# Kernel tuning notes

Hardware: AMD Instinct MI355X
Metric: run time of the kernel (lower is better)

## Reference

```python
import jax, jax.numpy as jnp
import numpy as np

NUM_IMU = 72
NUM_NOISE = 12
MAX_PROP = 300
LN_EPS = 1e-5

def _softplus(x):
    return jax.nn.softplus(x)

def setup_inputs() -> dict:
    key = jax.random.key(0)
    k1, k2, k3, k4, k5 = jax.random.split(key, 5)
    d_model = 1024
    seq_len = 4096
    hidden_states = jax.random.normal(k1, (1, seq_len, d_model), dtype=jnp.float32)
    ln_gamma = jnp.ones((d_model,), dtype=jnp.float32)
    ln_beta = jnp.zeros((d_model,), dtype=jnp.float32)
    # Linear: d_model -> NUM_IMU * NUM_NOISE
    W = jax.random.normal(k2, (d_model, NUM_IMU * NUM_NOISE), dtype=jnp.float32) / np.sqrt(d_model)
    b = jax.random.normal(k3, (NUM_IMU * NUM_NOISE,), dtype=jnp.float32) * 0.01
    return {"hidden_states": hidden_states, "ln_gamma": ln_gamma, "ln_beta": ln_beta, "W": W, "b": b}

def _forward(hidden_states, ln_gamma, ln_beta, W, b):
    seq_len = hidden_states.shape[1]
    tsteps = min(MAX_PROP, seq_len)
    x = hidden_states[0]  # [seq, d_model] (squeeze batch=1)
    mu = jnp.mean(x, axis=-1, keepdims=True)
    var = jnp.mean((x - mu) ** 2, axis=-1, keepdims=True)
    xn = (x - mu) * jax.lax.rsqrt(var + LN_EPS) * ln_gamma + ln_beta
    # noise params: [seq, NUM_NOISE, NUM_IMU]
    p = (xn @ W + b).reshape(seq_len, NUM_NOISE, NUM_IMU)
    c = p[:, 4, :]
    c_theta = p[:, 5, :]
    phi = p[:, 6, :]
    phi_theta = p[:, 7, :]
    d = _softplus(p[:, 1, :])
    k = d ** 2 / 4 + _softplus(p[:, 0, :])
    d_theta = _softplus(p[:, 3, :])
    k_theta = d_theta ** 2 / 4 + _softplus(p[:, 2, :])
    acc_base = p[:, 8, :].T      # [imu, seq]
    acc_std = _softplus(p[:, 9, :]).T
    gyro_base = p[:, 10, :].T
    gyro_std = _softplus(p[:, 11, :]).T
    # vectorize over imu: move to [imu, seq, 1]
    def I(a):
        return a.T[:, :, None]
    t = jnp.arange(tsteps, dtype=jnp.float32)[None, None, :]  # [1,1,tstep]
    k_, d_, phi_, c_ = I(k), I(d), I(phi), I(c)
    kt_, dt_, pht_, ct_ = I(k_theta), I(d_theta), I(phi_theta), I(c_theta)
    omega1 = jnp.sqrt(k_ * 4 - d_ ** 2) / 2
    lin = c_ * jnp.exp(-d_ / 2 * t) * jnp.sin(t * omega1 + phi_)
    omega2 = jnp.sqrt(kt_ * 4 - dt_ ** 2) / 2
    ang = ct_ * jnp.exp(-dt_ / 2 * t) * jnp.sin(t * omega2 + pht_)
    spring = lin + ang  # [imu, seq, tstep]
    # banded scatter-add: out[s+t] += spring[:, s, t] for s+t < seq_len
    pos = jnp.arange(seq_len, dtype=jnp.int32)[:, None] + jnp.arange(tsteps, dtype=jnp.int32)[None, :]
    pos_flat = pos.reshape(-1)
    mask = pos_flat < seq_len
    pos_safe = jnp.where(mask, pos_flat, 0)
    vals = spring.reshape(NUM_IMU, -1) * mask.astype(spring.dtype)
    kinematics = jnp.zeros((NUM_IMU, seq_len), dtype=spring.dtype).at[:, pos_safe].add(vals)
    return kinematics, acc_base, acc_std, gyro_base, gyro_std

def reference(hidden_states, ln_gamma, ln_beta, W, b):
    return _forward(hidden_states, ln_gamma, ln_beta, W, b)
```

## Files before the change

### kernel.cpp

```cpp
#include <hip/hip_runtime.h>
#include <hip/hip_bf16.h>
#include <math.h>

#define SEQ 4096
#define DM  1024
#define NIMU 72
#define NNOISE 12
#define NJ (NIMU*NNOISE)
#define TSTEPS 300
#define PLANE (NIMU*SEQ)

#define A2F_SHORTS ((size_t)256 * 64 * 512)
#define BTF_SHORTS ((size_t)56 * 64 * 512)

typedef __attribute__((ext_vector_type(8))) short bf16x8;
typedef __attribute__((ext_vector_type(4))) float f32x4;
typedef __attribute__((ext_vector_type(2))) float f32x2;

__device__ __forceinline__ float softplus_f(float x) {
    return fmaxf(x, 0.f) + log1pf(expf(-fabsf(x)));
}

__device__ __forceinline__ void split_bf16(float x, short& hi, short& lo) {
    unsigned b = __float_as_uint(x);
    unsigned h = (b + 0x7FFFu + ((b >> 16) & 1u)) >> 16;
    float hf = __uint_as_float(h << 16);
    float r = x - hf;
    unsigned b2 = __float_as_uint(r);
    unsigned l2 = (b2 + 0x7FFFu + ((b2 >> 16) & 1u)) >> 16;
    hi = (short)h;
    lo = (short)l2;
}

__global__ __launch_bounds__(256) void ln_kernel(const float* __restrict__ x,
                                                 const float* __restrict__ gamma,
                                                 const float* __restrict__ beta,
                                                 short* __restrict__ A2f) {
    const int s_tile = blockIdx.x;
    const int tid = threadIdx.x;
    const int mrow = tid >> 4;
    const int g    = tid & 15;
    const int row  = s_tile * 16 + mrow;
    const float4* xr = (const float4*)(x + (size_t)row * DM);

    float s = 0.f, sq = 0.f;
    #pragma unroll
    for (int i = 0; i < 16; ++i) {
        float4 v = xr[g + 16 * i];
        s  += v.x + v.y + v.z + v.w;
        sq += v.x*v.x + v.y*v.y + v.z*v.z + v.w*v.w;
    }
    #pragma unroll
    for (int off = 1; off < 16; off <<= 1) {
        s  += __shfl_xor(s, off);
        sq += __shfl_xor(sq, off);
    }
    const float mean = s * (1.f / DM);
    const float var  = sq * (1.f / DM) - mean * mean;
    const float rstd = rsqrtf(fmaxf(var, 0.f) + 1e-5f);

    #pragma unroll
    for (int i = 0; i < 16; ++i) {
        float4 v = xr[g + 16 * i];
        float4 gm = ((const float4*)gamma)[g + 16 * i];
        float4 bt = ((const float4*)beta)[g + 16 * i];
        float o[4];
        o[0] = (v.x - mean) * rstd * gm.x + bt.x;
        o[1] = (v.y - mean) * rstd * gm.y + bt.y;
        o[2] = (v.z - mean) * rstd * gm.z + bt.z;
        o[3] = (v.w - mean) * rstd * gm.w + bt.w;
        short4 hv, lv;
        split_bf16(o[0], hv.x, lv.x);
        split_bf16(o[1], hv.y, lv.y);
        split_bf16(o[2], hv.z, lv.z);
        split_bf16(o[3], hv.w, lv.w);
        const int ch = (g >> 3) + 2 * i;
        const size_t base = ((size_t)s_tile * 64 + ch) * 512
                          + mrow * 8 + ((g >> 1) & 3) * 128 + (g & 1) * 4;
        *(short4*)(A2f + base)             = hv;
        *(short4*)(A2f + base + 32 * 512)  = lv;
    }
}

__global__ __launch_bounds__(256) void wprep_kernel(const float* __restrict__ W,
                                                    short* __restrict__ Btf) {
    __shared__ float T[32][33];
    const int k0 = blockIdx.x * 32, j0 = blockIdx.y * 32;
    const int t = threadIdx.x;
    {
        const int r = t >> 3, c4 = (t & 7) * 4;
        float4 v = *(const float4*)(W + (size_t)(k0 + r) * NJ + j0 + c4);
        T[r][c4 + 0] = v.x; T[r][c4 + 1] = v.y; T[r][c4 + 2] = v.z; T[r][c4 + 3] = v.w;
    }
    __syncthreads();
    if (t < 128) {
        const int gq = t >> 6;
        const int l  = t & 63;
        const int n = l & 15, c = l >> 4;
        const int jt = blockIdx.y * 2 + gq;
        bf16x8 hv, lv;
        #pragma unroll
        for (int o = 0; o < 8; ++o) {
            short h, lo_;
            split_bf16(T[c * 8 + o][gq * 16 + n], h, lo_);
            hv[o] = h; lv[o] = lo_;
        }
        short* dh = Btf + ((size_t)jt * 64 + blockIdx.x) * 512 + l * 8;
        *(bf16x8*)dh = hv;
        *(bf16x8*)(dh + (size_t)32 * 512) = lv;
    }
}

__global__ __launch_bounds__(256, 1) void gemm_kernel(const short* __restrict__ A2f,
                                                      const short* __restrict__ Btf,
                                                      const float* __restrict__ bias,
                                                      float* __restrict__ pt) {
    const int l = threadIdx.x & 63, w = threadIdx.x >> 6;
    const int st0 = blockIdx.x * 8 + (w & 1) * 4;
    const int jt0 = blockIdx.y * 8 + (w >> 1) * 4;
    const short* aB = A2f + (size_t)st0 * (64 * 512) + l * 8;
    const short* bB = Btf + (size_t)jt0 * (64 * 512) + l * 8;

    f32x4 acc[4][4] = {};
    bf16x8 ah[2][4], al[2][4], bh[2][4], bl[2][4];

    auto ldstep = [&](int slot, int i) {
        #pragma unroll
        for (int t = 0; t < 4; ++t) {
            ah[slot][t] = *(const bf16x8*)(aB + ((size_t)t * 64 + i) * 512);
            al[slot][t] = *(const bf16x8*)(aB + ((size_t)t * 64 + 32 + i) * 512);
            bh[slot][t] = *(const bf16x8*)(bB + ((size_t)t * 64 + i) * 512);
            bl[slot][t] = *(const bf16x8*)(bB + ((size_t)t * 64 + 32 + i) * 512);
        }
    };

    ldstep(0, 0);
    #pragma unroll 2
    for (int i = 0; i < 32; ++i) {
        const int cur = i & 1;
        if (i + 1 < 32) ldstep(cur ^ 1, i + 1);
        #pragma unroll
        for (int mi = 0; mi < 4; ++mi)
            #pragma unroll
            for (int ni = 0; ni < 4; ++ni)
                acc[mi][ni] = __builtin_amdgcn_mfma_f32_16x16x32_bf16(
                    ah[cur][mi], bh[cur][ni], acc[mi][ni], 0, 0, 0);
        #pragma unroll
        for (int mi = 0; mi < 4; ++mi)
            #pragma unroll
            for (int ni = 0; ni < 4; ++ni)
                acc[mi][ni] = __builtin_amdgcn_mfma_f32_16x16x32_bf16(
                    ah[cur][mi], bl[cur][ni], acc[mi][ni], 0, 0, 0);
        #pragma unroll
        for (int mi = 0; mi < 4; ++mi)
            #pragma unroll
            for (int ni = 0; ni < 4; ++ni)
                acc[mi][ni] = __builtin_amdgcn_mfma_f32_16x16x32_bf16(
                    al[cur][mi], bh[cur][ni], acc[mi][ni], 0, 0, 0);
    }

    const int srow = (l >> 4) * 4;
    const int jcol = l & 15;
    #pragma unroll
    for (int ni = 0; ni < 4; ++ni) {
        const int j = (jt0 + ni) * 16 + jcol;
        if (j < NJ) {
            const float bj = bias[j];
            #pragma unroll
            for (int mi = 0; mi < 4; ++mi) {
                f32x4 v = acc[mi][ni];
                v[0] += bj; v[1] += bj; v[2] += bj; v[3] += bj;
                *(f32x4*)(pt + (size_t)j * SEQ + (st0 + mi) * 16 + srow) = v;
            }
        }
    }
}

__global__ __launch_bounds__(256) void spring_kernel(const float* __restrict__ pt,
                                                     float* __restrict__ kin) {
    const int tid  = threadIdx.x;
    const int lane = tid & 63;
    const int wid  = tid >> 6;
    const int s0   = blockIdx.x * 256;
    const int imu  = blockIdx.y;
    const int th   = blockIdx.z;
    const int tbeg = th ? 152 : 0;
    const int tlen = th ? 148 : 152;
    const int sbase = s0 + (wid << 6);
    const int s    = sbase + lane;

    const int base = imu * SEQ + s;
    const float p0  = pt[(size_t)0 * PLANE + base];
    const float p1  = pt[(size_t)1 * PLANE + base];
    const float p2  = pt[(size_t)2 * PLANE + base];
    const float p3  = pt[(size_t)3 * PLANE + base];
    const float c1  = pt[(size_t)4 * PLANE + base];
    const float c2  = pt[(size_t)5 * PLANE + base];
    const float ph1 = pt[(size_t)6 * PLANE + base];
    const float ph2 = pt[(size_t)7 * PLANE + base];

    float dd = softplus_f(p1);
    float kk = dd * dd * 0.25f + softplus_f(p0);
    float om1 = 0.5f * sqrtf(fmaxf(4.f * kk - dd * dd, 0.f));
    float dt = softplus_f(p3);
    float kt = dt * dt * 0.25f + softplus_f(p2);
    float om2 = 0.5f * sqrtf(fmaxf(4.f * kt - dt * dt, 0.f));
    float e1 = expf(-0.5f * dd), e2 = expf(-0.5f * dt);
    float sn, cs, sn2, cs2;
    sincosf(om1, &sn, &cs);
    sincosf(om2, &sn2, &cs2);
    f32x2 Rr = {e1 * cs, e2 * cs2};
    f32x2 Ri = {e1 * sn, e2 * sn2};
    sincosf(ph1, &sn, &cs);
    sincosf(ph2, &sn2, &cs2);
    f32x2 zr = {c1 * cs, c2 * cs2};
    f32x2 zi = {c1 * sn, c2 * sn2};

    if (th) {
        f32x2 prr = Rr, pri = Ri;
        f32x2 qr = {1.f, 1.f}, qi = {0.f, 0.f};
        int e = 152;
        while (e) {
            if (e & 1) {
                f32x2 nr = qr * prr - qi * pri;
                qi = qr * pri + qi * prr;
                qr = nr;
            }
            f32x2 nr = prr * prr - pri * pri;
            pri = 2.f * prr * pri;
            prr = nr;
            e >>= 1;
        }
        f32x2 nr = zr * qr - zi * qi;
        zi = zr * qi + zi * qr;
        zr = nr;
    }

    float A[4];
    #pragma unroll
    for (int r = 0; r < 4; ++r) A[r] = 0.f;

    const bool full = (sbase + 63 + tbeg + tlen - 1) < SEQ;

    if (full) {
        #pragma unroll
        for (int tq = 0; tq < 3; ++tq) {
            const int trmax = (tq == 2) ? (tlen - 128) : 64;
            for (int tr0 = 0; tr0 < trmax; tr0 += 4) {
                float v[4], u[4];
                #pragma unroll
                for (int i = 0; i < 4; ++i) {
                    v[i] = zi.x + zi.y;
                    f32x2 nr = zr * Rr - zi * Ri;
                    zi = zr * Ri + zi * Rr;
                    zr = nr;
                }
                #pragma unroll
                for (int i = 0; i < 4; ++i)
                    u[i] = __shfl(v[i], (lane - (tr0 + i)) & 63);
                #pragma unroll
                for (int i = 0; i < 4; ++i) {
                    const int tr = tr0 + i;
                    A[tq]     += (lane >= tr) ? u[i] : 0.f;
                    A[tq + 1] += (lane <  tr) ? u[i] : 0.f;
                }
            }
        }
    } else {
        const int tmax_lane = SEQ - s - tbeg;
        #pragma unroll
        for (int tq = 0; tq < 3; ++tq) {
            const int trmax = (tq == 2) ? (tlen - 128) : 64;
            for (int tr = 0; tr < trmax; ++tr) {
                const int t2 = tq * 64 + tr;
                float val = (t2 < tmax_lane) ? (zi.x + zi.y) : 0.f;
                float u = __shfl(val, (lane - tr) & 63);
                A[tq]     += (lane >= tr) ? u : 0.f;
                A[tq + 1] += (lane <  tr) ? u : 0.f;
                f32x2 nr = zr * Rr - zi * Ri;
                zi = zr * Ri + zi * Rr;
                zr = nr;
            }
        }
    }

    const int pbase = sbase + tbeg;
    #pragma unroll
    for (int r = 0; r < 4; ++r) {
        const int idx = r * 64 + lane;
        if (idx < tlen + 63) {
            const int pos = pbase + idx;
            if (pos < SEQ) {
                __hip_atomic_fetch_add(&kin[(size_t)imu * SEQ + pos], A[r],
                                       __ATOMIC_RELAXED, __HIP_MEMORY_SCOPE_AGENT);
            }
        }
    }
}

__global__ __launch_bounds__(256) void tail_kernel(const float* __restrict__ pt,
                                                   float* __restrict__ out) {
    int idx = blockIdx.x * 256 + threadIdx.x;
    if (idx >= 4 * PLANE) return;
    float v = pt[(size_t)8 * PLANE + idx];
    int q = idx / PLANE;
    if (q & 1) v = softplus_f(v);
    out[(size_t)PLANE + idx] = v;
}

extern "C" void kernel_launch(void* const* d_in, const int* in_sizes, int n_in,
                              void* d_out, int out_size, void* d_ws, size_t ws_size,
                              hipStream_t stream) {
    const float* hs    = (const float*)d_in[0];
    const float* gamma = (const float*)d_in[1];
    const float* beta  = (const float*)d_in[2];
    const float* W     = (const float*)d_in[3];
    const float* b     = (const float*)d_in[4];
    float* out = (float*)d_out;

    short* A2f = (short*)d_ws;
    short* Btf = A2f + A2F_SHORTS;
    float* pt  = (float*)(Btf + BTF_SHORTS);

    hipMemsetAsync(out, 0, (size_t)PLANE * sizeof(float), stream);

    ln_kernel<<<SEQ / 16, 256, 0, stream>>>(hs, gamma, beta, A2f);
    wprep_kernel<<<dim3(DM / 32, NJ / 32), 256, 0, stream>>>(W, Btf);
    gemm_kernel<<<dim3(SEQ / 128, 7), 256, 0, stream>>>(A2f, Btf, b, pt);
    spring_kernel<<<dim3(SEQ / 256, NIMU, 2), 256, 0, stream>>>(pt, out);
    tail_kernel<<<(4 * PLANE + 255) / 256, 256, 0, stream>>>(pt, out);
}
```

Measured before the change: 159.8 us.

## Fuse tail outputs into GEMM epilogue and restructure spring kernel into persistent tiles

The GEMM epilogue now writes the acc/gyro base and std planes straight to the output, applying softplus where needed, which removes the separate tail kernel and its round trip through the workspace. The spring kernel becomes a persistent grid of 1536 blocks looping over 4608 virtual tiles, with the time range split into four chunks of about 76 steps instead of two of about 150. Each chunk uses a 2-accumulator scheme with incrementally updated ds_bpermute indices in place of __shfl. Splitting time four ways adds more atomics and more power-by-squaring setup per tile, in exchange for more parallelism and shorter serial recurrences.

```diff
diff --git a/kernel.cpp b/kernel.cpp
--- a/kernel.cpp
+++ b/kernel.cpp
@@ -114,7 +114,8 @@
 __global__ __launch_bounds__(256, 1) void gemm_kernel(const short* __restrict__ A2f,
                                                       const short* __restrict__ Btf,
                                                       const float* __restrict__ bias,
-                                                      float* __restrict__ pt) {
+                                                      float* __restrict__ pt,
+                                                      float* __restrict__ out) {
     const int l = threadIdx.x & 63, w = threadIdx.x >> 6;
     const int st0 = blockIdx.x * 8 + (w & 1) * 4;
     const int jt0 = blockIdx.y * 8 + (w >> 1) * 4;
@@ -166,146 +167,166 @@
         const int j = (jt0 + ni) * 16 + jcol;
         if (j < NJ) {
             const float bj = bias[j];
-            #pragma unroll
-            for (int mi = 0; mi < 4; ++mi) {
-                f32x4 v = acc[mi][ni];
-                v[0] += bj; v[1] += bj; v[2] += bj; v[3] += bj;
-                *(f32x4*)(pt + (size_t)j * SEQ + (st0 + mi) * 16 + srow) = v;
+            if (j < 8 * NIMU) {
+                #pragma unroll
+                for (int mi = 0; mi < 4; ++mi) {
+                    f32x4 v = acc[mi][ni];
+                    v[0] += bj; v[1] += bj; v[2] += bj; v[3] += bj;
+                    *(f32x4*)(pt + (size_t)j * SEQ + (st0 + mi) * 16 + srow) = v;
+                }
+            } else {
+                const int q  = (j - 8 * NIMU) / NIMU;
+                const int im = (j - 8 * NIMU) - NIMU * q;
+                float* dst = out + (size_t)(1 + q) * PLANE + (size_t)im * SEQ;
+                #pragma unroll
+                for (int mi = 0; mi < 4; ++mi) {
+                    f32x4 v = acc[mi][ni];
+                    v[0] += bj; v[1] += bj; v[2] += bj; v[3] += bj;
+                    if (q & 1) {
+                        v[0] = softplus_f(v[0]); v[1] = softplus_f(v[1]);
+                        v[2] = softplus_f(v[2]); v[3] = softplus_f(v[3]);
+                    }
+                    *(f32x4*)(dst + (st0 + mi) * 16 + srow) = v;
+                }
             }
         }
     }
 }
+
+#define NVTILE 4608
+#define PGRID  1536
 
 __global__ __launch_bounds__(256) void spring_kernel(const float* __restrict__ pt,
                                                      float* __restrict__ kin) {
     const int tid  = threadIdx.x;
     const int lane = tid & 63;
     const int wid  = tid >> 6;
-    const int s0   = blockIdx.x * 256;
-    const int imu  = blockIdx.y;
-    const int th   = blockIdx.z;
-    const int tbeg = th ? 152 : 0;
-    const int tlen = th ? 148 : 152;
-    const int sbase = s0 + (wid << 6);
-    const int s    = sbase + lane;
-
-    const int base = imu * SEQ + s;
-    const float p0  = pt[(size_t)0 * PLANE + base];
-    const float p1  = pt[(size_t)1 * PLANE + base];
-    const float p2  = pt[(size_t)2 * PLANE + base];
-    const float p3  = pt[(size_t)3 * PLANE + base];
-    const float c1  = pt[(size_t)4 * PLANE + base];
-    const float c2  = pt[(size_t)5 * PLANE + base];
-    const float ph1 = pt[(size_t)6 * PLANE + base];
-    const float ph2 = pt[(size_t)7 * PLANE + base];
-
-    float dd = softplus_f(p1);
-    float kk = dd * dd * 0.25f + softplus_f(p0);
-    float om1 = 0.5f * sqrtf(fmaxf(4.f * kk - dd * dd, 0.f));
-    float dt = softplus_f(p3);
-    float kt = dt * dt * 0.25f + softplus_f(p2);
-    float om2 = 0.5f * sqrtf(fmaxf(4.f * kt - dt * dt, 0.f));
-    float e1 = expf(-0.5f * dd), e2 = expf(-0.5f * dt);
-    float sn, cs, sn2, cs2;
-    sincosf(om1, &sn, &cs);
-    sincosf(om2, &sn2, &cs2);
-    f32x2 Rr = {e1 * cs, e2 * cs2};
-    f32x2 Ri = {e1 * sn, e2 * sn2};
-    sincosf(ph1, &sn, &cs);
-    sincosf(ph2, &sn2, &cs2);
-    f32x2 zr = {c1 * cs, c2 * cs2};
-    f32x2 zi = {c1 * sn, c2 * sn2};
-
-    if (th) {
-        f32x2 prr = Rr, pri = Ri;
-        f32x2 qr = {1.f, 1.f}, qi = {0.f, 0.f};
-        int e = 152;
-        while (e) {
-            if (e & 1) {
-                f32x2 nr = qr * prr - qi * pri;
-                qi = qr * pri + qi * prr;
-                qr = nr;
+
+    for (int vt = blockIdx.x; vt < NVTILE; vt += PGRID) {
+        const int tc   = vt & 3;
+        const int rr   = vt >> 2;
+        const int imu  = rr % NIMU;
+        const int sblk = rr / NIMU;
+        const int tbeg = 76 * tc;
+        const int tlen = (tc == 3) ? 72 : 76;
+        const int sbase = sblk * 256 + (wid << 6);
+        const int s    = sbase + lane;
+
+        const int base = imu * SEQ + s;
+        const float p0  = pt[(size_t)0 * PLANE + base];
+        const float p1  = pt[(size_t)1 * PLANE + base];
+        const float p2  = pt[(size_t)2 * PLANE + base];
+        const float p3  = pt[(size_t)3 * PLANE + base];
+        const float c1  = pt[(size_t)4 * PLANE + base];
+        const float c2  = pt[(size_t)5 * PLANE + base];
+        const float ph1 = pt[(size_t)6 * PLANE + base];
+        const float ph2 = pt[(size_t)7 * PLANE + base];
+
+        float dd = softplus_f(p1);
+        float kk = dd * dd * 0.25f + softplus_f(p0);
+        float om1 = 0.5f * sqrtf(fmaxf(4.f * kk - dd * dd, 0.f));
+        float dt = softplus_f(p3);
+        float kt = dt * dt * 0.25f + softplus_f(p2);
+        float om2 = 0.5f * sqrtf(fmaxf(4.f * kt - dt * dt, 0.f));
+        float e1 = expf(-0.5f * dd), e2 = expf(-0.5f * dt);
+        float sn, cs, sn2, cs2;
+        sincosf(om1, &sn, &cs);
+        sincosf(om2, &sn2, &cs2);
+        const f32x2 Rr = {e1 * cs, e2 * cs2};
+        const f32x2 Ri = {e1 * sn, e2 * sn2};
+        sincosf(ph1, &sn, &cs);
+        sincosf(ph2, &sn2, &cs2);
+        f32x2 zr = {c1 * cs, c2 * cs2};
+        f32x2 zi = {c1 * sn, c2 * sn2};
+
+        if (tbeg) {
+            f32x2 prr = Rr, pri = Ri;
+            f32x2 qr = {1.f, 1.f}, qi = {0.f, 0.f};
+            int e = tbeg;
+            while (e) {
+                if (e & 1) {
+                    f32x2 nr = qr * prr - qi * pri;
+                    qi = qr * pri + qi * prr;
+                    qr = nr;
+                }
+                f32x2 nr = prr * prr - pri * pri;
+                pri = 2.f * prr * pri;
+                prr = nr;
+                e >>= 1;
             }
-            f32x2 nr = prr * prr - pri * pri;
-            pri = 2.f * prr * pri;
-            prr = nr;
-            e >>= 1;
-        }
-        f32x2 nr = zr * qr - zi * qi;
-        zi = zr * qi + zi * qr;
-        zr = nr;
-    }
-
-    float A[4];
-    #pragma unroll
-    for (int r = 0; r < 4; ++r) A[r] = 0.f;
-
-    const bool full = (sbase + 63 + tbeg + tlen - 1) < SEQ;
-
-    if (full) {
-        #pragma unroll
-        for (int tq = 0; tq < 3; ++tq) {
-            const int trmax = (tq == 2) ? (tlen - 128) : 64;
-            for (int tr0 = 0; tr0 < trmax; tr0 += 4) {
-                float v[4], u[4];
-                #pragma unroll
-                for (int i = 0; i < 4; ++i) {
-                    v[i] = zi.x + zi.y;
-                    f32x2 nr = zr * Rr - zi * Ri;
-                    zi = zr * Ri + zi * Rr;
-                    zr = nr;
-                }
-                #pragma unroll
-                for (int i = 0; i < 4; ++i)
-                    u[i] = __shfl(v[i], (lane - (tr0 + i)) & 63);
-                #pragma unroll
-                for (int i = 0; i < 4; ++i) {
-                    const int tr = tr0 + i;
-                    A[tq]     += (lane >= tr) ? u[i] : 0.f;
-                    A[tq + 1] += (lane <  tr) ? u[i] : 0.f;
-                }
-            }
-        }
-    } else {
+            f32x2 nr = zr * qr - zi * qi;
+            zi = zr * qi + zi * qr;
+            zr = nr;
+        }
+
+        float A0 = 0.f, A1 = 0.f, A2v = 0.f;
+        int idx0 = ( lane      & 63) << 2;
+        int idx1 = ((lane - 1) & 63) << 2;
+        int idx2 = ((lane - 2) & 63) << 2;
+        int idx3 = ((lane - 3) & 63) << 2;
+
+        const bool full = (sbase + 63 + tbeg + tlen - 1) < SEQ;
         const int tmax_lane = SEQ - s - tbeg;
-        #pragma unroll
-        for (int tq = 0; tq < 3; ++tq) {
-            const int trmax = (tq == 2) ? (tlen - 128) : 64;
-            for (int tr = 0; tr < trmax; ++tr) {
-                const int t2 = tq * 64 + tr;
-                float val = (t2 < tmax_lane) ? (zi.x + zi.y) : 0.f;
-                float u = __shfl(val, (lane - tr) & 63);
-                A[tq]     += (lane >= tr) ? u : 0.f;
-                A[tq + 1] += (lane <  tr) ? u : 0.f;
-                f32x2 nr = zr * Rr - zi * Ri;
-                zi = zr * Ri + zi * Rr;
-                zr = nr;
-            }
-        }
-    }
-
-    const int pbase = sbase + tbeg;
-    #pragma unroll
-    for (int r = 0; r < 4; ++r) {
-        const int idx = r * 64 + lane;
-        if (idx < tlen + 63) {
-            const int pos = pbase + idx;
-            if (pos < SEQ) {
-                __hip_atomic_fetch_add(&kin[(size_t)imu * SEQ + pos], A[r],
-                                       __ATOMIC_RELAXED, __HIP_MEMORY_SCOPE_AGENT);
-            }
-        }
-    }
-}
-
-__global__ __launch_bounds__(256) void tail_kernel(const float* __restrict__ pt,
-                                                   float* __restrict__ out) {
-    int idx = blockIdx.x * 256 + threadIdx.x;
-    if (idx >= 4 * PLANE) return;
-    float v = pt[(size_t)8 * PLANE + idx];
-    int q = idx / PLANE;
-    if (q & 1) v = softplus_f(v);
-    out[(size_t)PLANE + idx] = v;
+
+        #define ADV() { f32x2 nr_ = zr * Rr - zi * Ri;             \
+                        zi = zr * Ri + zi * Rr; zr = nr_; }
+        #define BPERM(u_, v_) u_ = __int_as_float(                 \
+            __builtin_amdgcn_ds_bpermute(idx##u_##_, __float_as_int(v_)))
+
+        #define CHUNK(AL, AH, TQ, TRMAX, MASKED)                                  \
+        {                                                                         \
+            float B = 0.f, C = 0.f;                                               \
+            for (int tr0 = 0; tr0 < (TRMAX); tr0 += 4) {                          \
+                float v0, v1, v2, v3;                                             \
+                v0 = zi.x + zi.y;                                                 \
+                if (MASKED) v0 = ((TQ)*64 + tr0 + 0 < tmax_lane) ? v0 : 0.f;      \
+                ADV();                                                            \
+                v1 = zi.x + zi.y;                                                 \
+                if (MASKED) v1 = ((TQ)*64 + tr0 + 1 < tmax_lane) ? v1 : 0.f;      \
+                ADV();                                                            \
+                v2 = zi.x + zi.y;                                                 \
+                if (MASKED) v2 = ((TQ)*64 + tr0 + 2 < tmax_lane) ? v2 : 0.f;      \
+                ADV();                                                            \
+                v3 = zi.x + zi.y;                                                 \
+                if (MASKED) v3 = ((TQ)*64 + tr0 + 3 < tmax_lane) ? v3 : 0.f;      \
+                ADV();                                                            \
+                float u0 = __int_as_float(__builtin_amdgcn_ds_bpermute(idx0, __float_as_int(v0))); \
+                float u1 = __int_as_float(__builtin_amdgcn_ds_bpermute(idx1, __float_as_int(v1))); \
+                float u2 = __int_as_float(__builtin_amdgcn_ds_bpermute(idx2, __float_as_int(v2))); \
+                float u3 = __int_as_float(__builtin_amdgcn_ds_bpermute(idx3, __float_as_int(v3))); \
+                idx0 = (idx0 - 16) & 252; idx1 = (idx1 - 16) & 252;               \
+                idx2 = (idx2 - 16) & 252; idx3 = (idx3 - 16) & 252;               \
+                B += u0; C += (lane < tr0 + 0) ? u0 : 0.f;                        \
+                B += u1; C += (lane < tr0 + 1) ? u1 : 0.f;                        \
+                B += u2; C += (lane < tr0 + 2) ? u2 : 0.f;                        \
+                B += u3; C += (lane < tr0 + 3) ? u3 : 0.f;                        \
+            }                                                                     \
+            AL += B - C; AH += C;                                                 \
+        }
+
+        const int trmax2 = tlen - 64;
+        if (full) {
+            CHUNK(A0, A1, 0, 64, 0)
+            CHUNK(A1, A2v, 1, trmax2, 0)
+        } else {
+            CHUNK(A0, A1, 0, 64, 1)
+            CHUNK(A1, A2v, 1, trmax2, 1)
+        }
+        #undef CHUNK
+        #undef ADV
+
+        const int pbase = sbase + tbeg;
+        float* kimu = kin + (size_t)imu * SEQ;
+        int pos = pbase + lane;
+        if (pos < SEQ)
+            __hip_atomic_fetch_add(kimu + pos, A0, __ATOMIC_RELAXED, __HIP_MEMORY_SCOPE_AGENT);
+        pos += 64;
+        if (pos < SEQ)
+            __hip_atomic_fetch_add(kimu + pos, A1, __ATOMIC_RELAXED, __HIP_MEMORY_SCOPE_AGENT);
+        pos += 64;
+        if (lane <= tlen - 66 && pos < SEQ)
+            __hip_atomic_fetch_add(kimu + pos, A2v, __ATOMIC_RELAXED, __HIP_MEMORY_SCOPE_AGENT);
+    }
 }
 
 extern "C" void kernel_launch(void* const* d_in, const int* in_sizes, int n_in,
@@ -326,7 +347,6 @@
 
     ln_kernel<<<SEQ / 16, 256, 0, stream>>>(hs, gamma, beta, A2f);
     wprep_kernel<<<dim3(DM / 32, NJ / 32), 256, 0, stream>>>(W, Btf);
-    gemm_kernel<<<dim3(SEQ / 128, 7), 256, 0, stream>>>(A2f, Btf, b, pt);
-    spring_kernel<<<dim3(SEQ / 256, NIMU, 2), 256, 0, stream>>>(pt, out);
-    tail_kernel<<<(4 * PLANE + 255) / 256, 256, 0, stream>>>(pt, out);
-}
+    gemm_kernel<<<dim3(SEQ / 128, 7), 256, 0, stream>>>(A2f, Btf, b, pt, out);
+    spring_kernel<<<PGRID, 256, 0, stream>>>(pt, out);
+}
```

New measurement: 178.0 us. 11.4% more time.
